# Performance work log

Hardware: AMD Instinct MI355X
Metric: run time of the kernel (lower is better)

## Reference

```python
import jax, jax.numpy as jnp
import numpy as np

K = 5       # kernel_size
UP = 2      # up_factor
EPS = 1e-5  # BatchNorm eps (eval mode)


def _conv(x, w, pad, dil=1):
    return jax.lax.conv_general_dilated(
        x, w, (1, 1), [(pad, pad), (pad, pad)], rhs_dilation=(dil, dil),
        dimension_numbers=('NCHW', 'OIHW', 'NCHW'))


def _bn(x, g, b, m, v):
    inv = g / jnp.sqrt(v + EPS)
    return x * inv[:, None, None] + (b - m * inv)[:, None, None]


def _bilinear(x, oh, ow):
    # torch F.interpolate(mode='bilinear', align_corners=False)
    N, C, H, W = x.shape
    def coords(out_s, in_s):
        s = in_s / out_s
        src = (jnp.arange(out_s, dtype=jnp.float32) + 0.5) * s - 0.5
        src = jnp.clip(src, 0.0, in_s - 1)
        i0 = jnp.floor(src).astype(jnp.int32)
        i1 = jnp.minimum(i0 + 1, in_s - 1)
        return i0, i1, src - i0
    y0, y1, wy = coords(oh, H)
    x0, x1, wx = coords(ow, W)
    g = lambda yi, xi: x[:, :, yi][:, :, :, xi]  # (N,C,oh,ow)
    top = g(y0, x0) * (1 - wx) + g(y0, x1) * wx
    bot = g(y1, x0) * (1 - wx) + g(y1, x1) * wx
    return top * (1 - wy)[:, None] + bot * wy[:, None]


def _unfold(x):
    # F.unfold(k=5, pad=2) reshaped to (N, C, K*K, H, W); channel-major (c, kh, kw)
    p = K // 2
    N, C, H, W = x.shape
    xp = jnp.pad(x, ((0, 0), (0, 0), (p, p), (p, p)))
    patches = [xp[:, :, i:i + H, j:j + W] for i in range(K) for j in range(K)]
    return jnp.stack(patches, axis=2)


def setup_inputs() -> dict:
    key = jax.random.key(0)
    ks = jax.random.split(key, 8)
    N, C, H, W = 2, 256, 48, 48
    Cc = C // 4
    Cout = 256
    d = {}
    d['x'] = jax.random.normal(ks[0], (N, C, H, W), dtype=jnp.float32)
    d['compress_w'] = jax.random.normal(ks[1], (Cc, C, 1, 1), dtype=jnp.float32) * 0.05
    d['g1'] = jnp.ones((Cc,), jnp.float32)
    d['b1'] = jnp.zeros((Cc,), jnp.float32)
    d['m1'] = jax.random.normal(ks[2], (Cc,), dtype=jnp.float32) * 0.1
    d['v1'] = jax.random.uniform(ks[3], (Cc,), minval=0.5, maxval=1.5, dtype=jnp.float32)
    d['ke1_w'] = jax.random.normal(ks[4], (Cc, Cc, 3, 3), dtype=jnp.float32) * 0.05
    d['gk'] = jnp.ones((Cc,), jnp.float32)
    d['bk'] = jnp.zeros((Cc,), jnp.float32)
    d['mk'] = jax.random.normal(ks[5], (Cc,), dtype=jnp.float32) * 0.1
    d['vk'] = jax.random.uniform(ks[6], (Cc,), minval=0.5, maxval=1.5, dtype=jnp.float32)
    d['ke2_w'] = jax.random.normal(ks[7], (UP * UP * K * K, Cc, 3, 3), dtype=jnp.float32) * 0.05
    d['proj_w'] = jax.random.normal(jax.random.fold_in(key, 10), (Cout, C, 1, 1), dtype=jnp.float32) * 0.05
    d['g2'] = jnp.ones((Cout,), jnp.float32)
    d['b2'] = jnp.zeros((Cout,), jnp.float32)
    d['m2'] = jax.random.normal(jax.random.fold_in(key, 11), (Cout,), dtype=jnp.float32) * 0.1
    d['v2'] = jax.random.uniform(jax.random.fold_in(key, 12), (Cout,), minval=0.5, maxval=1.5, dtype=jnp.float32)
    return d


def reference(x, compress_w, g1, b1, m1, v1, ke1_w, gk, bk, mk, vk, ke2_w,
              proj_w, g2, b2, m2, v2):
    N, C, H, W = x.shape
    oh, ow = H * UP, W * UP
    # kernel prediction branch
    comp = jax.nn.relu(_bn(_conv(x, compress_w, 0), g1, b1, m1, v1))
    k1 = jax.nn.relu(_bn(_conv(comp, ke1_w, 2, dil=2), gk, bk, mk, vk))
    kernel = _conv(k1, ke2_w, 1)                               # (N, UP^2*K^2, H, W)
    kernel = jax.nn.softmax(kernel.reshape(N, UP * UP, K * K, H, W), axis=2)
    # content reassembly
    x_up = jnp.repeat(jnp.repeat(x, UP, axis=2), UP, axis=3)
    x_unf = _unfold(x_up)                                      # (N, C, K^2, oh, ow)
    k_up = _bilinear(kernel.reshape(N, UP * UP * K * K, H, W), oh, ow)
    k_up = k_up.reshape(N, UP * UP, K * K, oh, ow)
    out = jnp.einsum('nckhw,nukhw->nuchw', x_unf, k_up)        # (N, UP^2, C, oh, ow)
    # view (N, UP^2*C, oh, ow) then pixel_shuffle(UP)
    out = out.reshape(N, UP * UP * C, oh, ow)
    out = out.reshape(N, C, UP, UP, oh, ow)
    out = out.transpose(0, 1, 4, 2, 5, 3).reshape(N, C, oh * UP, ow * UP)
    out = jax.nn.relu(_bn(_conv(out, proj_w, 0), g2, b2, m2, v2))
    return out
```

## Files before the change

kernel.cpp:

```cpp
#include <hip/hip_runtime.h>

#define EPSB 1e-5f

typedef __attribute__((ext_vector_type(8))) short bf16x8;
typedef __attribute__((ext_vector_type(4))) float f32x4;

__device__ __forceinline__ unsigned short f2b(float f) {
  union { float f; unsigned u; } cv; cv.f = f;
  unsigned r = cv.u + 0x7FFFu + ((cv.u >> 16) & 1u);
  return (unsigned short)(r >> 16);
}

__global__ __launch_bounds__(256) void k_prep(
    const float* __restrict__ pw, const float* __restrict__ cw,
    const float* __restrict__ k1w, const float* __restrict__ k2w,
    const float* __restrict__ g1, const float* __restrict__ b1,
    const float* __restrict__ m1, const float* __restrict__ v1,
    const float* __restrict__ gk, const float* __restrict__ bk,
    const float* __restrict__ mk, const float* __restrict__ vk,
    const float* __restrict__ g2, const float* __restrict__ b2,
    const float* __restrict__ m2, const float* __restrict__ v2,
    unsigned short* __restrict__ pwb, unsigned short* __restrict__ wcb_t,
    unsigned short* __restrict__ wt1, unsigned short* __restrict__ wt2,
    float* __restrict__ sb1, float* __restrict__ sbk, float* __restrict__ sb2) {
  int i = blockIdx.x * 256 + threadIdx.x;
  if (i < 65536) pwb[i] = f2b(pw[i]);
  int j = i - 65536;
  if (j >= 0 && j < 16384) { int ci = j >> 6, co = j & 63; wcb_t[j] = f2b(cw[co * 256 + ci]); }
  int a = i - 81920;
  if (a >= 0 && a < 36864) {
    int co = a / 576, k = a % 576, tap = k >> 6, ci = k & 63;
    wt1[a] = f2b(k1w[co * 576 + ci * 9 + tap]);
  }
  int c2 = i - 118784;
  if (c2 >= 0 && c2 < 73728) {
    int co = c2 / 576, k = c2 % 576, tap = k >> 6, ci = k & 63;
    wt2[c2] = (co < 100) ? f2b(k2w[co * 576 + ci * 9 + tap]) : (unsigned short)0;
  }
  int s = i - 192512;
  if (s >= 0 && s < 64) { float iv = g1[s] / sqrtf(v1[s] + EPSB); sb1[s] = iv; sb1[64 + s] = b1[s] - m1[s] * iv; }
  if (s >= 64 && s < 128) { int c = s - 64; float iv = gk[c] / sqrtf(vk[c] + EPSB); sbk[c] = iv; sbk[64 + c] = bk[c] - mk[c] * iv; }
  if (s >= 128 && s < 384) { int c = s - 128; float iv = g2[c] / sqrtf(v2[c] + EPSB); sb2[c] = iv; sb2[256 + c] = b2[c] - m2[c] * iv; }
}

__global__ __launch_bounds__(256) void k_compress(
    const float* __restrict__ x, const unsigned short* __restrict__ wcb_t,
    const float* __restrict__ sb1, unsigned short* __restrict__ comp_t) {
  __shared__ unsigned short wl[16384];
  int t = threadIdx.x;
  for (int f = t; f < 2048; f += 256)
    *(bf16x8*)&wl[f * 8] = *(const bf16x8*)&wcb_t[f * 8];
  __syncthreads();
  int idx = blockIdx.x * 256 + t;
  int co2 = (idx & 31) * 2;
  int pg = idx >> 5;
  int n = pg / 1152;
  int pix0 = (pg % 1152) * 2;
  const float* xp = x + (size_t)n * 256 * 2304 + pix0;
  float a00 = 0.f, a01 = 0.f, a10 = 0.f, a11 = 0.f;
  for (int ci = 0; ci < 256; ++ci) {
    float2 xv = *(const float2*)(xp + (size_t)ci * 2304);
    unsigned pr = *(const unsigned*)&wl[ci * 64 + co2];
    union { unsigned u; float f; } wa, wb;
    wa.u = pr << 16; wb.u = pr & 0xffff0000u;
    a00 = fmaf(xv.x, wa.f, a00); a01 = fmaf(xv.y, wa.f, a01);
    a10 = fmaf(xv.x, wb.f, a10); a11 = fmaf(xv.y, wb.f, a11);
  }
  float s0 = sb1[co2], s1 = sb1[co2 + 1];
  float c0b = sb1[64 + co2], c1b = sb1[64 + co2 + 1];
  float o00 = fmaxf(fmaf(a00, s0, c0b), 0.f), o01 = fmaxf(fmaf(a01, s0, c0b), 0.f);
  float o10 = fmaxf(fmaf(a10, s1, c1b), 0.f), o11 = fmaxf(fmaf(a11, s1, c1b), 0.f);
  int r = pix0 / 48, c = pix0 % 48;
  unsigned short* ob = comp_t + ((size_t)n * 2704 + (r + 2) * 52 + (c + 2)) * 64 + co2;
  unsigned p0 = (unsigned)f2b(o00) | ((unsigned)f2b(o10) << 16);
  unsigned p1 = (unsigned)f2b(o01) | ((unsigned)f2b(o11) << 16);
  *(unsigned*)&ob[0]  = p0;
  *(unsigned*)&ob[64] = p1;
}

__global__ __launch_bounds__(256) void k_ke1(
    const unsigned short* __restrict__ comp_t, const unsigned short* __restrict__ wt1,
    const float* __restrict__ sbk, unsigned short* __restrict__ k1_t) {
  __shared__ unsigned short sA[16640];
  int t = threadIdx.x;
  int bid = blockIdx.x;
  int n = bid / 48, y = bid % 48;
  const unsigned short* src = comp_t + ((size_t)n * 52 + y) * 52 * 64;
  for (int f = t; f < 2080; f += 256) {
    int g = f >> 3, ci0 = (f & 7) * 8;
    int cc = g % 52, rr = g / 52;
    bf16x8 vv = *(const bf16x8*)&src[(rr * 52 + cc) * 64 + ci0];
    int ba = (((rr * 52 + cc) * 64 + ci0) * 2) ^ ((cc & 7) << 4);
    *(bf16x8*)((char*)sA + ba) = vv;
  }
  __syncthreads();
  int wid = t >> 6, l = t & 63, l15 = l & 15, lg = l >> 4;
  f32x4 acc[3];
  acc[0] = acc[1] = acc[2] = (f32x4){0.f, 0.f, 0.f, 0.f};
  const unsigned short* arow = wt1 + (size_t)(wid * 16 + l15) * 576;
#pragma unroll
  for (int kbi = 0; kbi < 18; ++kbi) {
    int tap = kbi >> 1;
    int ky = tap / 3, kx = tap % 3;
    int ci0 = (kbi & 1) * 32 + lg * 8;
    bf16x8 afr = *(const bf16x8*)&arow[kbi * 32 + lg * 8];
#pragma unroll
    for (int nt = 0; nt < 3; ++nt) {
      int col = nt * 16 + l15 + 2 * kx;
      int ba = (((2 * ky * 52 + col) * 64 + ci0) * 2) ^ ((col & 7) << 4);
      bf16x8 bfr = *(const bf16x8*)((char*)sA + ba);
      acc[nt] = __builtin_amdgcn_mfma_f32_16x16x32_bf16(afr, bfr, acc[nt], 0, 0, 0);
    }
  }
  unsigned short* dst = k1_t + ((size_t)n * 50 + (y + 1)) * 50 * 64;
  int co0 = wid * 16 + lg * 4;
  float s0 = sbk[co0], s1 = sbk[co0 + 1], s2 = sbk[co0 + 2], s3 = sbk[co0 + 3];
  float d0 = sbk[64 + co0], d1 = sbk[64 + co0 + 1], d2 = sbk[64 + co0 + 2], d3 = sbk[64 + co0 + 3];
#pragma unroll
  for (int nt = 0; nt < 3; ++nt) {
    int px = nt * 16 + l15;
    ushort4 pk;
    pk.x = f2b(fmaxf(fmaf(acc[nt][0], s0, d0), 0.f));
    pk.y = f2b(fmaxf(fmaf(acc[nt][1], s1, d1), 0.f));
    pk.z = f2b(fmaxf(fmaf(acc[nt][2], s2, d2), 0.f));
    pk.w = f2b(fmaxf(fmaf(acc[nt][3], s3, d3), 0.f));
    *(ushort4*)&dst[(px + 1) * 64 + co0] = pk;
  }
}

__global__ __launch_bounds__(256) void k_ke2(
    const unsigned short* __restrict__ k1_t, const unsigned short* __restrict__ wt2,
    float* __restrict__ kern_t) {
  __shared__ unsigned short sA[9600];
  int t = threadIdx.x;
  int bid = blockIdx.x;
  int n = bid / 48, y = bid % 48;
  const unsigned short* src = k1_t + ((size_t)n * 50 + y) * 50 * 64;
  for (int f = t; f < 1200; f += 256) {
    int g = f >> 3, ci0 = (f & 7) * 8;
    int cc = g % 50, rr = g / 50;
    bf16x8 vv = *(const bf16x8*)&src[(rr * 50 + cc) * 64 + ci0];
    int ba = (((rr * 50 + cc) * 64 + ci0) * 2) ^ ((cc & 7) << 4);
    *(bf16x8*)((char*)sA + ba) = vv;
  }
  __syncthreads();
  int wid = t >> 6, l = t & 63, l15 = l & 15, lg = l >> 4;
  f32x4 acc[2][3];
#pragma unroll
  for (int mi = 0; mi < 2; ++mi)
#pragma unroll
    for (int nt = 0; nt < 3; ++nt) acc[mi][nt] = (f32x4){0.f, 0.f, 0.f, 0.f};
#pragma unroll
  for (int kbi = 0; kbi < 18; ++kbi) {
    int tap = kbi >> 1;
    int ky = tap / 3, kx = tap % 3;
    int ci0 = (kbi & 1) * 32 + lg * 8;
    bf16x8 afr[2];
#pragma unroll
    for (int mi = 0; mi < 2; ++mi)
      afr[mi] = *(const bf16x8*)&wt2[(size_t)((wid * 2 + mi) * 16 + l15) * 576 + kbi * 32 + lg * 8];
#pragma unroll
    for (int nt = 0; nt < 3; ++nt) {
      int col = nt * 16 + l15 + kx;
      int ba = (((ky * 50 + col) * 64 + ci0) * 2) ^ ((col & 7) << 4);
      bf16x8 bfr = *(const bf16x8*)((char*)sA + ba);
      acc[0][nt] = __builtin_amdgcn_mfma_f32_16x16x32_bf16(afr[0], bfr, acc[0][nt], 0, 0, 0);
      acc[1][nt] = __builtin_amdgcn_mfma_f32_16x16x32_bf16(afr[1], bfr, acc[1][nt], 0, 0, 0);
    }
  }
#pragma unroll
  for (int mi = 0; mi < 2; ++mi) {
    int co0 = (wid * 2 + mi) * 16 + lg * 4;
    if (co0 < 100) {
#pragma unroll
      for (int nt = 0; nt < 3; ++nt) {
        int px = nt * 16 + l15;
        float4 vv = {acc[mi][nt][0], acc[mi][nt][1], acc[mi][nt][2], acc[mi][nt][3]};
        *(float4*)&kern_t[((size_t)n * 2304 + y * 48 + px) * 112 + co0] = vv;
      }
    }
  }
}

__global__ __launch_bounds__(256) void k_w9sm(const float* __restrict__ kern_t,
                                              float* __restrict__ w9) {
  int idx = blockIdx.x * 256 + threadIdx.x;
  int u = idx & 3;
  int w2 = (idx >> 2) % 96;
  int rest = (idx >> 2) / 96;
  int y96 = rest % 96;
  int n = rest / 96;
  float syf = fminf(fmaxf(y96 * 0.5f - 0.25f, 0.f), 47.f);
  int y0 = (int)syf; int y1 = min(y0 + 1, 47); float wy = syf - (float)y0;
  float sxf = fminf(fmaxf(w2 * 0.5f - 0.25f, 0.f), 47.f);
  int x0 = (int)sxf; int x1 = min(x0 + 1, 47); float wx = sxf - (float)x0;
  float bl[25];
#pragma unroll
  for (int k = 0; k < 25; ++k) bl[k] = 0.f;
  float ws4[4] = {(1.f - wx) * (1.f - wy), wx * (1.f - wy), (1.f - wx) * wy, wx * wy};
  int sy[4] = {y0, y0, y1, y1};
  int sx[4] = {x0, x1, x0, x1};
#pragma unroll
  for (int s = 0; s < 4; ++s) {
    const float* p = kern_t + ((size_t)n * 2304 + sy[s] * 48 + sx[s]) * 112 + u * 25;
    float vv[25], mx = -3.4e38f;
#pragma unroll
    for (int k = 0; k < 25; ++k) { vv[k] = p[k]; mx = fmaxf(mx, vv[k]); }
    float sum = 0.f;
#pragma unroll
    for (int k = 0; k < 25; ++k) { vv[k] = __expf(vv[k] - mx); sum += vv[k]; }
    float rs = ws4[s] / sum;
#pragma unroll
    for (int k = 0; k < 25; ++k) bl[k] = fmaf(vv[k], rs, bl[k]);
  }
#pragma unroll
  for (int kh = 0; kh < 5; ++kh) {
    bool vy = (unsigned)(y96 + kh - 2) < 96u;
#pragma unroll
    for (int kw = 0; kw < 5; ++kw) {
      bool vx = (unsigned)(w2 + kw - 2) < 96u;
      if (!(vy && vx)) bl[kh * 5 + kw] = 0.f;
    }
  }
  int py = y96 & 1, px_ = w2 & 1;
  float cc0[5], cc1[5], cc2[5];
#pragma unroll
  for (int kh = 0; kh < 5; ++kh) {
    cc0[kh] = px_ ? bl[kh * 5 + 0] : bl[kh * 5 + 0] + bl[kh * 5 + 1];
    cc1[kh] = px_ ? bl[kh * 5 + 1] + bl[kh * 5 + 2] : bl[kh * 5 + 2] + bl[kh * 5 + 3];
    cc2[kh] = px_ ? bl[kh * 5 + 3] + bl[kh * 5 + 4] : bl[kh * 5 + 4];
  }
  float* op = w9 + (((size_t)(n * 96 + y96) * 96 + w2) * 4 + u) * 9;
  op[0] = py ? cc0[0] : cc0[0] + cc0[1];
  op[1] = py ? cc1[0] : cc1[0] + cc1[1];
  op[2] = py ? cc2[0] : cc2[0] + cc2[1];
  op[3] = py ? cc0[1] + cc0[2] : cc0[2] + cc0[3];
  op[4] = py ? cc1[1] + cc1[2] : cc1[2] + cc1[3];
  op[5] = py ? cc2[1] + cc2[2] : cc2[2] + cc2[3];
  op[6] = py ? cc0[3] + cc0[4] : cc0[4];
  op[7] = py ? cc1[3] + cc1[4] : cc1[4];
  op[8] = py ? cc2[3] + cc2[4] : cc2[4];
}

__global__ __launch_bounds__(512) void k_reassemble_proj(
    const float* __restrict__ x, const float* __restrict__ w9,
    const unsigned short* __restrict__ pwb, const float* __restrict__ sb2,
    float* __restrict__ out) {
  __shared__ float xls[256 * 35];
  __shared__ float w9s[1152];
  __shared__ float sb2s[512];
  __shared__ unsigned short finT[128 * 256];

  int blk = blockIdx.x;
  int n = blk / 288;
  int r = blk % 288;
  int y48 = r / 6;
  int xt = r % 6;
  int X0 = xt * 32;
  int x480 = xt * 8;
  int t = threadIdx.x;

  sb2s[t] = sb2[t];
  {
    const float* base = w9 + ((size_t)(n * 96 + 2 * y48) * 96 + xt * 16) * 36;
    for (int f = t; f < 1152; f += 512) {
      int half = f / 576, o = f - half * 576;
      w9s[f] = base[(size_t)half * 3456 + o];
    }
  }
  const float* xb = x + (size_t)n * 256 * 2304;
  for (int f = t; f < 8448; f += 512) {
    int c = f / 33, rc = f - c * 33;
    int ry = rc / 11, cx = rc - ry * 11;
    int sy = min(max(y48 + ry - 1, 0), 47);
    int sx = min(max(x480 + cx - 1, 0), 47);
    int slot = (c & 3) * 64 + (c >> 2);
    xls[slot * 35 + rc] = xb[(size_t)c * 2304 + sy * 48 + sx];
  }
  __syncthreads();

  {
    int ci = t & 255;
    int half = t >> 8;
    int u = ci >> 6, ch = ci & 63;
    int cb = ci >> 3, crr = ci & 7;
#pragma unroll
    for (int rY = 0; rY < 2; ++rY) {
      int Yl = half * 2 + rY;
      const float* xc0 = &xls[((rY * 2 + 0) * 64 + ch) * 35];
      const float* xc1 = &xls[((rY * 2 + 1) * 64 + ch) * 35];
      float xw0[9], xw1[9];
#pragma unroll
      for (int ry = 0; ry < 3; ++ry)
#pragma unroll
        for (int cx = 0; cx < 3; ++cx) {
          xw0[ry * 3 + cx] = xc0[ry * 11 + cx];
          xw1[ry * 3 + cx] = xc1[ry * 11 + cx];
        }
#pragma unroll
      for (int j = 0; j < 16; ++j) {
        if (j >= 2 && (j & 1) == 0) {
          int nc = (j >> 1) + 2;
#pragma unroll
          for (int ry = 0; ry < 3; ++ry) {
            xw0[ry*3+0]=xw0[ry*3+1]; xw0[ry*3+1]=xw0[ry*3+2]; xw0[ry*3+2]=xc0[ry*11+nc];
            xw1[ry*3+0]=xw1[ry*3+1]; xw1[ry*3+1]=xw1[ry*3+2]; xw1[ry*3+2]=xc1[ry*11+nc];
          }
        }
        const float* wt = &w9s[(half * 16 + j) * 36 + u * 9];
        float a0 = 0.f, a1 = 0.f;
#pragma unroll
        for (int k9 = 0; k9 < 9; ++k9) {
          float wv = wt[k9];
          a0 = fmaf(xw0[k9], wv, a0);
          a1 = fmaf(xw1[k9], wv, a1);
        }
        int px0 = Yl * 32 + 2 * j, px1 = px0 + 1;
        finT[px0 * 256 + ((cb ^ (px0 & 7)) * 8 + crr)] = f2b(a0);
        finT[px1 * 256 + ((cb ^ (px1 & 7)) * 8 + crr)] = f2b(a1);
      }
    }
  }
  __syncthreads();

  int wid = t >> 6, l = t & 63, l15 = l & 15, lg = l >> 4;
  f32x4 acc[2][8];
#pragma unroll
  for (int mi = 0; mi < 2; ++mi)
#pragma unroll
    for (int nt = 0; nt < 8; ++nt) acc[mi][nt] = (f32x4){0.f, 0.f, 0.f, 0.f};
  const unsigned short* a0p = pwb + (size_t)(wid * 2 * 16 + l15) * 256;
  const unsigned short* a1p = a0p + 16 * 256;
#pragma unroll
  for (int kbi = 0; kbi < 8; ++kbi) {
    bf16x8 afr0 = *(const bf16x8*)&a0p[kbi * 32 + lg * 8];
    bf16x8 afr1 = *(const bf16x8*)&a1p[kbi * 32 + lg * 8];
    int cbk = kbi * 4 + lg;
#pragma unroll
    for (int nt = 0; nt < 8; ++nt) {
      int row = nt * 16 + l15;
      bf16x8 bfr = *(const bf16x8*)&finT[row * 256 + ((cbk ^ (row & 7)) * 8)];
      acc[0][nt] = __builtin_amdgcn_mfma_f32_16x16x32_bf16(afr0, bfr, acc[0][nt], 0, 0, 0);
      acc[1][nt] = __builtin_amdgcn_mfma_f32_16x16x32_bf16(afr1, bfr, acc[1][nt], 0, 0, 0);
    }
  }
  size_t outn = (size_t)n * 256 * 36864;
  int Ybase = 4 * y48;
#pragma unroll
  for (int mi = 0; mi < 2; ++mi) {
    int mt = wid * 2 + mi;
#pragma unroll
    for (int r4 = 0; r4 < 4; ++r4) {
      int o = mt * 16 + lg * 4 + r4;
      float sc = sb2s[o], bi = sb2s[256 + o];
#pragma unroll
      for (int nt = 0; nt < 8; ++nt) {
        int px = nt * 16 + l15;
        int Yl = px >> 5, Xl = px & 31;
        float val = fmaxf(fmaf(acc[mi][nt][r4], sc, bi), 0.f);
        out[outn + (size_t)o * 36864 + (size_t)(Ybase + Yl) * 192 + X0 + Xl] = val;
      }
    }
  }
}

extern "C" void kernel_launch(void* const* d_in, const int* in_sizes, int n_in,
                              void* d_out, int out_size, void* d_ws, size_t ws_size,
                              hipStream_t stream) {
  const float* x   = (const float*)d_in[0];
  const float* cw  = (const float*)d_in[1];
  const float* g1  = (const float*)d_in[2];
  const float* b1  = (const float*)d_in[3];
  const float* m1  = (const float*)d_in[4];
  const float* v1  = (const float*)d_in[5];
  const float* k1w = (const float*)d_in[6];
  const float* gk  = (const float*)d_in[7];
  const float* bk  = (const float*)d_in[8];
  const float* mk  = (const float*)d_in[9];
  const float* vk  = (const float*)d_in[10];
  const float* k2w = (const float*)d_in[11];
  const float* pw  = (const float*)d_in[12];
  const float* g2  = (const float*)d_in[13];
  const float* b2  = (const float*)d_in[14];
  const float* m2  = (const float*)d_in[15];
  const float* v2  = (const float*)d_in[16];
  float* out = (float*)d_out;
  float* ws  = (float*)d_ws;

  unsigned short* comp_t = (unsigned short*)ws;
  unsigned short* k1_t   = (unsigned short*)(ws + 173056);
  float* kern_t = ws + 333056;
  float* w9     = ws + 849152;
  unsigned short* pwb   = (unsigned short*)(ws + 1512704);
  unsigned short* wcb_t = (unsigned short*)(ws + 1545472);
  unsigned short* wt1   = (unsigned short*)(ws + 1553664);
  unsigned short* wt2   = (unsigned short*)(ws + 1572096);
  float* sb1 = ws + 1608960;
  float* sbk = ws + 1609088;
  float* sb2 = ws + 1609216;

  hipMemsetAsync(comp_t, 0, 346112 * 2, stream);
  hipMemsetAsync(k1_t, 0, 320000 * 2, stream);

  k_prep<<<754, 256, 0, stream>>>(pw, cw, k1w, k2w, g1, b1, m1, v1,
                                  gk, bk, mk, vk, g2, b2, m2, v2,
                                  pwb, wcb_t, wt1, wt2, sb1, sbk, sb2);
  k_compress<<<288, 256, 0, stream>>>(x, wcb_t, sb1, comp_t);
  k_ke1<<<96, 256, 0, stream>>>(comp_t, wt1, sbk, k1_t);
  k_ke2<<<96, 256, 0, stream>>>(k1_t, wt2, kern_t);
  k_w9sm<<<288, 256, 0, stream>>>(kern_t, w9);
  k_reassemble_proj<<<576, 512, 0, stream>>>(x, w9, pwb, sb2, out);
}
```

Measured before the change: 211.1 us.

## Fold workspace zeroing into prep, stage w9sm in LDS, split reassembly into chunks

The two hipMemsetAsync calls are removed and the zeroing of the padded comp/k1 buffers moves into the prep kernel, which saves launches. The softmax/bilinear kernel now gives each block one source row triple staged in LDS, so the four neighbour reads per output hit shared memory instead of global. The reassembly+projection kernel processes two 64-pixel chunks in sequence, which halves the finT LDS buffer and the accumulator registers, with launch_bounds(512,4) added to raise occupancy. The cost is extra barriers, serialized chunks, and only 96 blocks for w9sm.

```diff
diff --git a/kernel.cpp b/kernel.cpp
--- a/kernel.cpp
+++ b/kernel.cpp
@@ -22,8 +22,10 @@
     const float* __restrict__ m2, const float* __restrict__ v2,
     unsigned short* __restrict__ pwb, unsigned short* __restrict__ wcb_t,
     unsigned short* __restrict__ wt1, unsigned short* __restrict__ wt2,
-    float* __restrict__ sb1, float* __restrict__ sbk, float* __restrict__ sb2) {
+    float* __restrict__ sb1, float* __restrict__ sbk, float* __restrict__ sb2,
+    float* __restrict__ wsz) {
   int i = blockIdx.x * 256 + threadIdx.x;
+  if (i < 333056) wsz[i] = 0.f;
   if (i < 65536) pwb[i] = f2b(pw[i]);
   int j = i - 65536;
   if (j >= 0 && j < 16384) { int ci = j >> 6, co = j & 63; wcb_t[j] = f2b(cw[co * 256 + ci]); }
@@ -184,72 +186,90 @@
 
 __global__ __launch_bounds__(256) void k_w9sm(const float* __restrict__ kern_t,
                                               float* __restrict__ w9) {
-  int idx = blockIdx.x * 256 + threadIdx.x;
-  int u = idx & 3;
-  int w2 = (idx >> 2) % 96;
-  int rest = (idx >> 2) / 96;
-  int y96 = rest % 96;
-  int n = rest / 96;
-  float syf = fminf(fmaxf(y96 * 0.5f - 0.25f, 0.f), 47.f);
-  int y0 = (int)syf; int y1 = min(y0 + 1, 47); float wy = syf - (float)y0;
-  float sxf = fminf(fmaxf(w2 * 0.5f - 0.25f, 0.f), 47.f);
-  int x0 = (int)sxf; int x1 = min(x0 + 1, 47); float wx = sxf - (float)x0;
-  float bl[25];
-#pragma unroll
-  for (int k = 0; k < 25; ++k) bl[k] = 0.f;
-  float ws4[4] = {(1.f - wx) * (1.f - wy), wx * (1.f - wy), (1.f - wx) * wy, wx * wy};
-  int sy[4] = {y0, y0, y1, y1};
-  int sx[4] = {x0, x1, x0, x1};
-#pragma unroll
-  for (int s = 0; s < 4; ++s) {
-    const float* p = kern_t + ((size_t)n * 2304 + sy[s] * 48 + sx[s]) * 112 + u * 25;
-    float vv[25], mx = -3.4e38f;
-#pragma unroll
-    for (int k = 0; k < 25; ++k) { vv[k] = p[k]; mx = fmaxf(mx, vv[k]); }
-    float sum = 0.f;
-#pragma unroll
-    for (int k = 0; k < 25; ++k) { vv[k] = __expf(vv[k] - mx); sum += vv[k]; }
-    float rs = ws4[s] / sum;
-#pragma unroll
-    for (int k = 0; k < 25; ++k) bl[k] = fmaf(vv[k], rs, bl[k]);
-  }
-#pragma unroll
-  for (int kh = 0; kh < 5; ++kh) {
-    bool vy = (unsigned)(y96 + kh - 2) < 96u;
-#pragma unroll
-    for (int kw = 0; kw < 5; ++kw) {
-      bool vx = (unsigned)(w2 + kw - 2) < 96u;
-      if (!(vy && vx)) bl[kh * 5 + kw] = 0.f;
-    }
-  }
-  int py = y96 & 1, px_ = w2 & 1;
-  float cc0[5], cc1[5], cc2[5];
-#pragma unroll
-  for (int kh = 0; kh < 5; ++kh) {
-    cc0[kh] = px_ ? bl[kh * 5 + 0] : bl[kh * 5 + 0] + bl[kh * 5 + 1];
-    cc1[kh] = px_ ? bl[kh * 5 + 1] + bl[kh * 5 + 2] : bl[kh * 5 + 2] + bl[kh * 5 + 3];
-    cc2[kh] = px_ ? bl[kh * 5 + 3] + bl[kh * 5 + 4] : bl[kh * 5 + 4];
-  }
-  float* op = w9 + (((size_t)(n * 96 + y96) * 96 + w2) * 4 + u) * 9;
-  op[0] = py ? cc0[0] : cc0[0] + cc0[1];
-  op[1] = py ? cc1[0] : cc1[0] + cc1[1];
-  op[2] = py ? cc2[0] : cc2[0] + cc2[1];
-  op[3] = py ? cc0[1] + cc0[2] : cc0[2] + cc0[3];
-  op[4] = py ? cc1[1] + cc1[2] : cc1[2] + cc1[3];
-  op[5] = py ? cc2[1] + cc2[2] : cc2[2] + cc2[3];
-  op[6] = py ? cc0[3] + cc0[4] : cc0[4];
-  op[7] = py ? cc1[3] + cc1[4] : cc1[4];
-  op[8] = py ? cc2[3] + cc2[4] : cc2[4];
-}
-
-__global__ __launch_bounds__(512) void k_reassemble_proj(
+  __shared__ float ks[3 * 48 * 116];
+  int bid = blockIdx.x;
+  int n = bid / 48, k = bid % 48;
+  int t = threadIdx.x;
+  int rows[3] = {max(k - 1, 0), k, min(k + 1, 47)};
+#pragma unroll
+  for (int s = 0; s < 3; ++s) {
+    const float* src = kern_t + ((size_t)n * 2304 + rows[s] * 48) * 112;
+    for (int f = t; f < 1344; f += 256) {
+      float4 vv = *(const float4*)&src[f * 4];
+      int sx = f / 28, c = (f % 28) * 4;
+      *(float4*)&ks[(s * 48 + sx) * 116 + c] = vv;
+    }
+  }
+  __syncthreads();
+#pragma unroll
+  for (int it = 0; it < 3; ++it) {
+    int f = t + it * 256;
+    int half = f / 384, rem = f % 384;
+    int w2 = rem >> 2, u = rem & 3;
+    int y96 = 2 * k + half;
+    float syf = fminf(fmaxf(y96 * 0.5f - 0.25f, 0.f), 47.f);
+    int y0 = (int)syf; int y1 = min(y0 + 1, 47); float wy = syf - (float)y0;
+    int sl0 = (y0 == k) ? 1 : 0;
+    int sl1 = (y1 == k) ? 1 : 2;
+    float sxf = fminf(fmaxf(w2 * 0.5f - 0.25f, 0.f), 47.f);
+    int x0 = (int)sxf; int x1 = min(x0 + 1, 47); float wx = sxf - (float)x0;
+    float bl[25];
+#pragma unroll
+    for (int kk = 0; kk < 25; ++kk) bl[kk] = 0.f;
+    float ws4[4] = {(1.f - wx) * (1.f - wy), wx * (1.f - wy), (1.f - wx) * wy, wx * wy};
+    int ssy[4] = {sl0, sl0, sl1, sl1};
+    int ssx[4] = {x0, x1, x0, x1};
+#pragma unroll
+    for (int s = 0; s < 4; ++s) {
+      const float* p = &ks[(ssy[s] * 48 + ssx[s]) * 116 + u * 25];
+      float vv[25], mx = -3.4e38f;
+#pragma unroll
+      for (int kk = 0; kk < 25; ++kk) { vv[kk] = p[kk]; mx = fmaxf(mx, vv[kk]); }
+      float sum = 0.f;
+#pragma unroll
+      for (int kk = 0; kk < 25; ++kk) { vv[kk] = __expf(vv[kk] - mx); sum += vv[kk]; }
+      float rs = ws4[s] / sum;
+#pragma unroll
+      for (int kk = 0; kk < 25; ++kk) bl[kk] = fmaf(vv[kk], rs, bl[kk]);
+    }
+#pragma unroll
+    for (int kh = 0; kh < 5; ++kh) {
+      bool vy = (unsigned)(y96 + kh - 2) < 96u;
+#pragma unroll
+      for (int kw = 0; kw < 5; ++kw) {
+        bool vx = (unsigned)(w2 + kw - 2) < 96u;
+        if (!(vy && vx)) bl[kh * 5 + kw] = 0.f;
+      }
+    }
+    int py = y96 & 1, px_ = w2 & 1;
+    float cc0[5], cc1[5], cc2[5];
+#pragma unroll
+    for (int kh = 0; kh < 5; ++kh) {
+      cc0[kh] = px_ ? bl[kh * 5 + 0] : bl[kh * 5 + 0] + bl[kh * 5 + 1];
+      cc1[kh] = px_ ? bl[kh * 5 + 1] + bl[kh * 5 + 2] : bl[kh * 5 + 2] + bl[kh * 5 + 3];
+      cc2[kh] = px_ ? bl[kh * 5 + 3] + bl[kh * 5 + 4] : bl[kh * 5 + 4];
+    }
+    float* op = w9 + (((size_t)(n * 96 + y96) * 96 + w2) * 4 + u) * 9;
+    op[0] = py ? cc0[0] : cc0[0] + cc0[1];
+    op[1] = py ? cc1[0] : cc1[0] + cc1[1];
+    op[2] = py ? cc2[0] : cc2[0] + cc2[1];
+    op[3] = py ? cc0[1] + cc0[2] : cc0[2] + cc0[3];
+    op[4] = py ? cc1[1] + cc1[2] : cc1[2] + cc1[3];
+    op[5] = py ? cc2[1] + cc2[2] : cc2[2] + cc2[3];
+    op[6] = py ? cc0[3] + cc0[4] : cc0[4];
+    op[7] = py ? cc1[3] + cc1[4] : cc1[4];
+    op[8] = py ? cc2[3] + cc2[4] : cc2[4];
+  }
+}
+
+__global__ __launch_bounds__(512, 4) void k_reassemble_proj(
     const float* __restrict__ x, const float* __restrict__ w9,
     const unsigned short* __restrict__ pwb, const float* __restrict__ sb2,
     float* __restrict__ out) {
   __shared__ float xls[256 * 35];
   __shared__ float w9s[1152];
   __shared__ float sb2s[512];
-  __shared__ unsigned short finT[128 * 256];
+  __shared__ unsigned short finT[64 * 256];
 
   int blk = blockIdx.x;
   int n = blk / 288;
@@ -279,14 +299,18 @@
   }
   __syncthreads();
 
-  {
-    int ci = t & 255;
-    int half = t >> 8;
-    int u = ci >> 6, ch = ci & 63;
-    int cb = ci >> 3, crr = ci & 7;
-#pragma unroll
-    for (int rY = 0; rY < 2; ++rY) {
-      int Yl = half * 2 + rY;
+  int ci = t & 255, rY = t >> 8;
+  int u = ci >> 6, ch = ci & 63;
+  int cb = ci >> 3, crr = ci & 7;
+  int wid = t >> 6, l = t & 63, l15 = l & 15, lg = l >> 4;
+  const unsigned short* a0p = pwb + (size_t)(wid * 2 * 16 + l15) * 256;
+  const unsigned short* a1p = a0p + 16 * 256;
+  size_t outn = (size_t)n * 256 * 36864;
+  int Ybase = 4 * y48;
+
+#pragma unroll
+  for (int chunk = 0; chunk < 2; ++chunk) {
+    {
       const float* xc0 = &xls[((rY * 2 + 0) * 64 + ch) * 35];
       const float* xc1 = &xls[((rY * 2 + 1) * 64 + ch) * 35];
       float xw0[9], xw1[9];
@@ -307,7 +331,7 @@
             xw1[ry*3+0]=xw1[ry*3+1]; xw1[ry*3+1]=xw1[ry*3+2]; xw1[ry*3+2]=xc1[ry*11+nc];
           }
         }
-        const float* wt = &w9s[(half * 16 + j) * 36 + u * 9];
+        const float* wt = &w9s[(chunk * 16 + j) * 36 + u * 9];
         float a0 = 0.f, a1 = 0.f;
 #pragma unroll
         for (int k9 = 0; k9 < 9; ++k9) {
@@ -315,52 +339,48 @@
           a0 = fmaf(xw0[k9], wv, a0);
           a1 = fmaf(xw1[k9], wv, a1);
         }
-        int px0 = Yl * 32 + 2 * j, px1 = px0 + 1;
+        int px0 = rY * 32 + 2 * j, px1 = px0 + 1;
         finT[px0 * 256 + ((cb ^ (px0 & 7)) * 8 + crr)] = f2b(a0);
         finT[px1 * 256 + ((cb ^ (px1 & 7)) * 8 + crr)] = f2b(a1);
       }
     }
-  }
-  __syncthreads();
-
-  int wid = t >> 6, l = t & 63, l15 = l & 15, lg = l >> 4;
-  f32x4 acc[2][8];
-#pragma unroll
-  for (int mi = 0; mi < 2; ++mi)
-#pragma unroll
-    for (int nt = 0; nt < 8; ++nt) acc[mi][nt] = (f32x4){0.f, 0.f, 0.f, 0.f};
-  const unsigned short* a0p = pwb + (size_t)(wid * 2 * 16 + l15) * 256;
-  const unsigned short* a1p = a0p + 16 * 256;
-#pragma unroll
-  for (int kbi = 0; kbi < 8; ++kbi) {
-    bf16x8 afr0 = *(const bf16x8*)&a0p[kbi * 32 + lg * 8];
-    bf16x8 afr1 = *(const bf16x8*)&a1p[kbi * 32 + lg * 8];
-    int cbk = kbi * 4 + lg;
-#pragma unroll
-    for (int nt = 0; nt < 8; ++nt) {
-      int row = nt * 16 + l15;
-      bf16x8 bfr = *(const bf16x8*)&finT[row * 256 + ((cbk ^ (row & 7)) * 8)];
-      acc[0][nt] = __builtin_amdgcn_mfma_f32_16x16x32_bf16(afr0, bfr, acc[0][nt], 0, 0, 0);
-      acc[1][nt] = __builtin_amdgcn_mfma_f32_16x16x32_bf16(afr1, bfr, acc[1][nt], 0, 0, 0);
-    }
-  }
-  size_t outn = (size_t)n * 256 * 36864;
-  int Ybase = 4 * y48;
-#pragma unroll
-  for (int mi = 0; mi < 2; ++mi) {
-    int mt = wid * 2 + mi;
-#pragma unroll
-    for (int r4 = 0; r4 < 4; ++r4) {
-      int o = mt * 16 + lg * 4 + r4;
-      float sc = sb2s[o], bi = sb2s[256 + o];
-#pragma unroll
-      for (int nt = 0; nt < 8; ++nt) {
-        int px = nt * 16 + l15;
-        int Yl = px >> 5, Xl = px & 31;
-        float val = fmaxf(fmaf(acc[mi][nt][r4], sc, bi), 0.f);
-        out[outn + (size_t)o * 36864 + (size_t)(Ybase + Yl) * 192 + X0 + Xl] = val;
+    __syncthreads();
+
+    f32x4 acc[2][4];
+#pragma unroll
+    for (int mi = 0; mi < 2; ++mi)
+#pragma unroll
+      for (int nt = 0; nt < 4; ++nt) acc[mi][nt] = (f32x4){0.f, 0.f, 0.f, 0.f};
+#pragma unroll
+    for (int kbi = 0; kbi < 8; ++kbi) {
+      bf16x8 afr0 = *(const bf16x8*)&a0p[kbi * 32 + lg * 8];
+      bf16x8 afr1 = *(const bf16x8*)&a1p[kbi * 32 + lg * 8];
+      int cbk = kbi * 4 + lg;
+#pragma unroll
+      for (int nt = 0; nt < 4; ++nt) {
+        int row = nt * 16 + l15;
+        bf16x8 bfr = *(const bf16x8*)&finT[row * 256 + ((cbk ^ (row & 7)) * 8)];
+        acc[0][nt] = __builtin_amdgcn_mfma_f32_16x16x32_bf16(afr0, bfr, acc[0][nt], 0, 0, 0);
+        acc[1][nt] = __builtin_amdgcn_mfma_f32_16x16x32_bf16(afr1, bfr, acc[1][nt], 0, 0, 0);
       }
     }
+#pragma unroll
+    for (int mi = 0; mi < 2; ++mi) {
+      int mt = wid * 2 + mi;
+#pragma unroll
+      for (int r4 = 0; r4 < 4; ++r4) {
+        int o = mt * 16 + lg * 4 + r4;
+        float sc = sb2s[o], bi = sb2s[256 + o];
+#pragma unroll
+        for (int nt = 0; nt < 4; ++nt) {
+          int px = nt * 16 + l15;
+          int Yl = chunk * 2 + (px >> 5), Xl = px & 31;
+          float val = fmaxf(fmaf(acc[mi][nt][r4], sc, bi), 0.f);
+          out[outn + (size_t)o * 36864 + (size_t)(Ybase + Yl) * 192 + X0 + Xl] = val;
+        }
+      }
+    }
+    __syncthreads();
   }
 }
 
@@ -399,15 +419,12 @@
   float* sbk = ws + 1609088;
   float* sb2 = ws + 1609216;
 
-  hipMemsetAsync(comp_t, 0, 346112 * 2, stream);
-  hipMemsetAsync(k1_t, 0, 320000 * 2, stream);
-
-  k_prep<<<754, 256, 0, stream>>>(pw, cw, k1w, k2w, g1, b1, m1, v1,
-                                  gk, bk, mk, vk, g2, b2, m2, v2,
-                                  pwb, wcb_t, wt1, wt2, sb1, sbk, sb2);
+  k_prep<<<1302, 256, 0, stream>>>(pw, cw, k1w, k2w, g1, b1, m1, v1,
+                                   gk, bk, mk, vk, g2, b2, m2, v2,
+                                   pwb, wcb_t, wt1, wt2, sb1, sbk, sb2, ws);
   k_compress<<<288, 256, 0, stream>>>(x, wcb_t, sb1, comp_t);
   k_ke1<<<96, 256, 0, stream>>>(comp_t, wt1, sbk, k1_t);
   k_ke2<<<96, 256, 0, stream>>>(k1_t, wt2, kern_t);
-  k_w9sm<<<288, 256, 0, stream>>>(kern_t, w9);
+  k_w9sm<<<96, 256, 0, stream>>>(kern_t, w9);
   k_reassemble_proj<<<576, 512, 0, stream>>>(x, w9, pwb, sb2, out);
 }
```

New measurement: 202.0 us. 4.3% less time.
